# Performance work log

Hardware: AMD Instinct MI355X
Metric: run time of the kernel (lower is better)

The kernel has to match this reference:

```python
import jax, jax.numpy as jnp
import numpy as np

E, T, A, H = 64, 128, 32, 4
S, O, QH1, QD, C1 = 256, 128, 128, 64, 128  # state, obs, query hidden, query/key dim, c hidden


def setup_inputs() -> dict:
    key = jax.random.key(0)
    ks = jax.random.split(key, 10)
    w = 0.02
    return {
        "q_values": jax.random.normal(ks[0], (E, T, A), jnp.float32),
        "states": jax.random.normal(ks[1], (E, T, S), jnp.float32),
        "individual_fs": jax.random.normal(ks[2], (E, T, A, O), jnp.float32),
        "Wq1": jax.random.normal(ks[3], (S, QH1), jnp.float32) * w,
        "bq1": jnp.zeros((QH1,), jnp.float32),
        "Wq2": jax.random.normal(ks[4], (QH1, QD), jnp.float32) * w,
        "bq2": jnp.zeros((QD,), jnp.float32),
        "Wk": jax.random.normal(ks[5], (H, O, QD), jnp.float32) * w,
        "bk": jnp.zeros((H, QD), jnp.float32),
        "Wc1": jax.random.normal(ks[6], (S, C1), jnp.float32) * w,
        "bc1": jnp.zeros((C1,), jnp.float32),
        "Wc2": jax.random.normal(ks[7], (C1, 1), jnp.float32) * w,
        "bc2": jnp.zeros((1,), jnp.float32),
    }


def reference(q_values, states, individual_fs, Wq1, bq1, Wq2, bq2, Wk, bk, Wc1, bc1, Wc2, bc2):
    e, t, a = q_values.shape
    s = states.reshape(-1, states.shape[-1])              # (B, S), B = E*T
    f = individual_fs.reshape(e * t, a, -1)               # (B, A, O)
    # query embedding of state: 2-layer MLP with ReLU
    emb_s = jnp.maximum(s @ Wq1 + bq1, 0.0) @ Wq2 + bq2   # (B, QD)
    # all-agents, all-heads key extraction in one batched einsum
    emb_u = jnp.einsum('bao,hok->bahk', f, Wk) + bk       # (B, A, H, QD)
    # query-key dot products per agent/head, then sum over heads
    Lambda_i = jnp.einsum('bk,bahk->bah', emb_s, emb_u).sum(axis=-1)  # (B, A)
    # state-dependent scalar bias
    c_value = jnp.maximum(s @ Wc1 + bc1, 0.0) @ Wc2 + bc2  # (B, 1)
    Q_tot = jnp.sum(Lambda_i * q_values.reshape(-1, a), axis=-1, keepdims=True) + c_value
    return Q_tot.reshape(e, t, 1)
```

## Files before the change

### kernel.cpp

```cpp
#include <hip/hip_runtime.h>


static constexpr int Sd  = 256;
static constexpr int Ad  = 32;
static constexpr int Od  = 128;
static constexpr int QDd = 64;
static constexpr int NB  = 8;
static constexpr int NBLK = 1024;

__global__ void qatten_prep(const float* __restrict__ Wk, const float* __restrict__ bk,
                            float* __restrict__ WkT, float* __restrict__ bkSum)
{
    int idx = blockIdx.x * 256 + threadIdx.x;
    int k = idx >> 7;
    int o = idx & 127;
    float s = 0.f;
#pragma unroll
    for (int h = 0; h < 4; ++h) s += Wk[h * (Od * QDd) + o * QDd + k];
    WkT[k * Od + o] = s;
    if (idx < QDd) {
        float t = 0.f;
#pragma unroll
        for (int h = 0; h < 4; ++h) t += bk[h * QDd + idx];
        bkSum[idx] = t;
    }
}

union SEmb {
    float s[NB][Sd];
    float emb[NB][68];
};

__global__ __launch_bounds__(256, 5) void qatten_fused(
    const float* __restrict__ qv, const float* __restrict__ st, const float* __restrict__ fs,
    const float* __restrict__ Wq1, const float* __restrict__ bq1,
    const float* __restrict__ Wq2, const float* __restrict__ bq2,
    const float* __restrict__ Wc1, const float* __restrict__ bc1,
    const float* __restrict__ Wc2, const float* __restrict__ bc2,
    const float* __restrict__ WkT, const float* __restrict__ bkSum,
    float* __restrict__ out)
{
    __shared__ SEmb u;
    __shared__ float h_lds[NB][260];
    __shared__ float g_lds[NB][128];

    const int tid = threadIdx.x;
    const int b0 = blockIdx.x * NB;

    {
        const int w = tid >> 6;
        const int l = tid & 63;
        const int r0 = b0 + 2 * w;
        const float4* __restrict__ f0 = (const float4*)fs + (size_t)r0 * (Ad * Od / 4);
        const float4* __restrict__ f1 = f0 + (Ad * Od / 4);
        const float q0 = qv[(size_t)r0 * Ad + (l & 31)];
        const float q1 = qv[(size_t)(r0 + 1) * Ad + (l & 31)];
        float4 a0 = {0.f, 0.f, 0.f, 0.f}, a1 = {0.f, 0.f, 0.f, 0.f};
#pragma unroll
        for (int batch = 0; batch < 2; ++batch) {
            float4 x0[8], x1[8];
#pragma unroll
            for (int i = 0; i < 8; ++i) {
                x0[i] = f0[(batch * 8 + i) * 64 + l];
                x1[i] = f1[(batch * 8 + i) * 64 + l];
            }
#pragma unroll
            for (int i = 0; i < 8; ++i) {
                const int ii = batch * 8 + i;
                const float qa0 = __shfl(q0, 2 * ii + (l >> 5), 64);
                const float qa1 = __shfl(q1, 2 * ii + (l >> 5), 64);
                a0.x = fmaf(qa0, x0[i].x, a0.x);
                a0.y = fmaf(qa0, x0[i].y, a0.y);
                a0.z = fmaf(qa0, x0[i].z, a0.z);
                a0.w = fmaf(qa0, x0[i].w, a0.w);
                a1.x = fmaf(qa1, x1[i].x, a1.x);
                a1.y = fmaf(qa1, x1[i].y, a1.y);
                a1.z = fmaf(qa1, x1[i].z, a1.z);
                a1.w = fmaf(qa1, x1[i].w, a1.w);
            }
        }
        a0.x += __shfl_xor(a0.x, 32, 64);
        a0.y += __shfl_xor(a0.y, 32, 64);
        a0.z += __shfl_xor(a0.z, 32, 64);
        a0.w += __shfl_xor(a0.w, 32, 64);
        a1.x += __shfl_xor(a1.x, 32, 64);
        a1.y += __shfl_xor(a1.y, 32, 64);
        a1.z += __shfl_xor(a1.z, 32, 64);
        a1.w += __shfl_xor(a1.w, 32, 64);
        if (l < 32) {
            *(float4*)&g_lds[2 * w][l * 4]     = a0;
            *(float4*)&g_lds[2 * w + 1][l * 4] = a1;
        }
    }

    {
        const float4* sp = (const float4*)(st + (size_t)b0 * Sd);
        float4* sl = (float4*)&u.s[0][0];
        sl[tid]       = sp[tid];
        sl[tid + 256] = sp[tid + 256];
    }
    __syncthreads();

    {
        const int wg = tid & 63;
        const int rg = (tid >> 6) << 1;
        const float* __restrict__ Wb = (wg < 32) ? (Wq1 + 4 * wg)
                                                 : (Wc1 + 4 * (wg - 32));
        const float4 bb4 = (wg < 32) ? *(const float4*)&bq1[4 * wg]
                                     : *(const float4*)&bc1[4 * (wg - 32)];
        float acc[2][4];
#pragma unroll
        for (int r = 0; r < 2; ++r)
#pragma unroll
            for (int c = 0; c < 4; ++c) acc[r][c] = 0.f;

        for (int k = 0; k < Sd; k += 4) {
            float w[4][4];
#pragma unroll
            for (int kk = 0; kk < 4; ++kk) {
                const float4 t = *(const float4*)&Wb[(size_t)(k + kk) * 128];
                w[kk][0] = t.x; w[kk][1] = t.y; w[kk][2] = t.z; w[kk][3] = t.w;
            }
#pragma unroll
            for (int r = 0; r < 2; ++r) {
                const float4 s4 = *(const float4*)&u.s[rg + r][k];
                float a0 = acc[r][0], a1 = acc[r][1], a2 = acc[r][2], a3 = acc[r][3];
                a0 = fmaf(s4.x, w[0][0], a0); a1 = fmaf(s4.x, w[0][1], a1);
                a2 = fmaf(s4.x, w[0][2], a2); a3 = fmaf(s4.x, w[0][3], a3);
                a0 = fmaf(s4.y, w[1][0], a0); a1 = fmaf(s4.y, w[1][1], a1);
                a2 = fmaf(s4.y, w[1][2], a2); a3 = fmaf(s4.y, w[1][3], a3);
                a0 = fmaf(s4.z, w[2][0], a0); a1 = fmaf(s4.z, w[2][1], a1);
                a2 = fmaf(s4.z, w[2][2], a2); a3 = fmaf(s4.z, w[2][3], a3);
                a0 = fmaf(s4.w, w[3][0], a0); a1 = fmaf(s4.w, w[3][1], a1);
                a2 = fmaf(s4.w, w[3][2], a2); a3 = fmaf(s4.w, w[3][3], a3);
                acc[r][0] = a0; acc[r][1] = a1; acc[r][2] = a2; acc[r][3] = a3;
            }
        }
#pragma unroll
        for (int r = 0; r < 2; ++r) {
            float4 o;
            o.x = fmaxf(acc[r][0] + bb4.x, 0.f);
            o.y = fmaxf(acc[r][1] + bb4.y, 0.f);
            o.z = fmaxf(acc[r][2] + bb4.z, 0.f);
            o.w = fmaxf(acc[r][3] + bb4.w, 0.f);
            *(float4*)&h_lds[rg + r][4 * wg] = o;
        }
    }
    __syncthreads();

    {
        const int c2  = tid & 31;
        const int row = tid >> 5;
        float a0 = 0.f, a1 = 0.f;
        for (int k = 0; k < 128; k += 4) {
            float2 w[4];
#pragma unroll
            for (int kk = 0; kk < 4; ++kk)
                w[kk] = *(const float2*)&Wq2[(size_t)(k + kk) * 64 + 2 * c2];
            const float4 h4 = *(const float4*)&h_lds[row][k];
            a0 = fmaf(h4.x, w[0].x, a0);  a1 = fmaf(h4.x, w[0].y, a1);
            a0 = fmaf(h4.y, w[1].x, a0);  a1 = fmaf(h4.y, w[1].y, a1);
            a0 = fmaf(h4.z, w[2].x, a0);  a1 = fmaf(h4.z, w[2].y, a1);
            a0 = fmaf(h4.w, w[3].x, a0);  a1 = fmaf(h4.w, w[3].y, a1);
        }
        const float2 b2 = *(const float2*)&bq2[2 * c2];
        float2 o; o.x = a0 + b2.x; o.y = a1 + b2.y;
        *(float2*)&u.emb[row][2 * c2] = o;
    }
    __syncthreads();

    {
        const int cg  = tid & 31;
        const int row = tid >> 5;
        const int b   = b0 + row;

        float acc[4] = {0.f, 0.f, 0.f, 0.f};
        for (int k = 0; k < QDd; k += 4) {
            float w[4][4];
#pragma unroll
            for (int kk = 0; kk < 4; ++kk) {
                const float4 t = *(const float4*)&WkT[(size_t)(k + kk) * 128 + 4 * cg];
                w[kk][0] = t.x; w[kk][1] = t.y; w[kk][2] = t.z; w[kk][3] = t.w;
            }
            const float4 e4 = *(const float4*)&u.emb[row][k];
#pragma unroll
            for (int c = 0; c < 4; ++c) {
                float a = acc[c];
                a = fmaf(e4.x, w[0][c], a);
                a = fmaf(e4.y, w[1][c], a);
                a = fmaf(e4.z, w[2][c], a);
                a = fmaf(e4.w, w[3][c], a);
                acc[c] = a;
            }
        }
        const float4 g4 = *(const float4*)&g_lds[row][4 * cg];
        float d = acc[0] * g4.x;
        d = fmaf(acc[1], g4.y, d);
        d = fmaf(acc[2], g4.z, d);
        d = fmaf(acc[3], g4.w, d);
        float pb = fmaf(u.emb[row][cg],      bkSum[cg],      0.f);
        pb       = fmaf(u.emb[row][cg + 32], bkSum[cg + 32], pb);
        float pc = 0.f;
#pragma unroll
        for (int j = 0; j < 4; ++j)
            pc = fmaf(h_lds[row][128 + cg + 32 * j], Wc2[cg + 32 * j], pc);
        float pq = qv[(size_t)b * Ad + cg];
#pragma unroll
        for (int dd = 16; dd >= 1; dd >>= 1) {
            d  += __shfl_down(d,  dd, 32);
            pb += __shfl_down(pb, dd, 32);
            pc += __shfl_down(pc, dd, 32);
            pq += __shfl_down(pq, dd, 32);
        }
        if (cg == 0)
            out[b] = d + (pc + bc2[0]) + pb * pq;
    }
}

extern "C" void kernel_launch(void* const* d_in, const int* in_sizes, int n_in,
                              void* d_out, int out_size, void* d_ws, size_t ws_size,
                              hipStream_t stream) {
    const float* qv  = (const float*)d_in[0];
    const float* st  = (const float*)d_in[1];
    const float* fs  = (const float*)d_in[2];
    const float* Wq1 = (const float*)d_in[3];
    const float* bq1 = (const float*)d_in[4];
    const float* Wq2 = (const float*)d_in[5];
    const float* bq2 = (const float*)d_in[6];
    const float* Wk  = (const float*)d_in[7];
    const float* bk  = (const float*)d_in[8];
    const float* Wc1 = (const float*)d_in[9];
    const float* bc1 = (const float*)d_in[10];
    const float* Wc2 = (const float*)d_in[11];
    const float* bc2 = (const float*)d_in[12];
    float* out = (float*)d_out;

    float* WkT   = (float*)d_ws;
    float* bkSum = WkT + QDd * Od;

    qatten_prep<<<32, 256, 0, stream>>>(Wk, bk, WkT, bkSum);
    qatten_fused<<<NBLK, 256, 0, stream>>>(qv, st, fs, Wq1, bq1, Wq2, bq2,
                                           Wc1, bc1, Wc2, bc2, WkT, bkSum, out);
}
```

Baseline: 269.9 us.

## Warp-specialize fused kernel: producer waves stream fs while compute waves run MLP

```diff
diff --git a/kernel.cpp b/kernel.cpp
--- a/kernel.cpp
+++ b/kernel.cpp
@@ -5,8 +5,8 @@
 static constexpr int Ad  = 32;
 static constexpr int Od  = 128;
 static constexpr int QDd = 64;
-static constexpr int NB  = 8;
-static constexpr int NBLK = 1024;
+static constexpr int NB  = 16;
+static constexpr int NBLK = 512;
 
 __global__ void qatten_prep(const float* __restrict__ Wk, const float* __restrict__ bk,
                             float* __restrict__ WkT, float* __restrict__ bkSum)
@@ -26,12 +26,7 @@
     }
 }
 
-union SEmb {
-    float s[NB][Sd];
-    float emb[NB][68];
-};
-
-__global__ __launch_bounds__(256, 5) void qatten_fused(
+__global__ __launch_bounds__(512) void qatten_fused(
     const float* __restrict__ qv, const float* __restrict__ st, const float* __restrict__ fs,
     const float* __restrict__ Wq1, const float* __restrict__ bq1,
     const float* __restrict__ Wq2, const float* __restrict__ bq2,
@@ -40,180 +35,190 @@
     const float* __restrict__ WkT, const float* __restrict__ bkSum,
     float* __restrict__ out)
 {
-    __shared__ SEmb u;
+    __shared__ float s_lds[NB][Sd];
     __shared__ float h_lds[NB][260];
+    __shared__ float emb_lds[NB][68];
     __shared__ float g_lds[NB][128];
 
-    const int tid = threadIdx.x;
-    const int b0 = blockIdx.x * NB;
-
-    {
-        const int w = tid >> 6;
-        const int l = tid & 63;
-        const int r0 = b0 + 2 * w;
-        const float4* __restrict__ f0 = (const float4*)fs + (size_t)r0 * (Ad * Od / 4);
-        const float4* __restrict__ f1 = f0 + (Ad * Od / 4);
-        const float q0 = qv[(size_t)r0 * Ad + (l & 31)];
-        const float q1 = qv[(size_t)(r0 + 1) * Ad + (l & 31)];
-        float4 a0 = {0.f, 0.f, 0.f, 0.f}, a1 = {0.f, 0.f, 0.f, 0.f};
-#pragma unroll
-        for (int batch = 0; batch < 2; ++batch) {
-            float4 x0[8], x1[8];
-#pragma unroll
-            for (int i = 0; i < 8; ++i) {
-                x0[i] = f0[(batch * 8 + i) * 64 + l];
-                x1[i] = f1[(batch * 8 + i) * 64 + l];
-            }
-#pragma unroll
-            for (int i = 0; i < 8; ++i) {
-                const int ii = batch * 8 + i;
-                const float qa0 = __shfl(q0, 2 * ii + (l >> 5), 64);
-                const float qa1 = __shfl(q1, 2 * ii + (l >> 5), 64);
-                a0.x = fmaf(qa0, x0[i].x, a0.x);
-                a0.y = fmaf(qa0, x0[i].y, a0.y);
-                a0.z = fmaf(qa0, x0[i].z, a0.z);
-                a0.w = fmaf(qa0, x0[i].w, a0.w);
-                a1.x = fmaf(qa1, x1[i].x, a1.x);
-                a1.y = fmaf(qa1, x1[i].y, a1.y);
-                a1.z = fmaf(qa1, x1[i].z, a1.z);
-                a1.w = fmaf(qa1, x1[i].w, a1.w);
-            }
-        }
-        a0.x += __shfl_xor(a0.x, 32, 64);
-        a0.y += __shfl_xor(a0.y, 32, 64);
-        a0.z += __shfl_xor(a0.z, 32, 64);
-        a0.w += __shfl_xor(a0.w, 32, 64);
-        a1.x += __shfl_xor(a1.x, 32, 64);
-        a1.y += __shfl_xor(a1.y, 32, 64);
-        a1.z += __shfl_xor(a1.z, 32, 64);
-        a1.w += __shfl_xor(a1.w, 32, 64);
-        if (l < 32) {
-            *(float4*)&g_lds[2 * w][l * 4]     = a0;
-            *(float4*)&g_lds[2 * w + 1][l * 4] = a1;
+    const int tid  = threadIdx.x;
+    const int wave = tid >> 6;
+    const int l    = tid & 63;
+    const int b0   = blockIdx.x * NB;
+
+    float vreg[4][2];
+
+    if (wave < 4) {
+        const int r0 = b0 + 4 * wave;
+#pragma unroll
+        for (int p = 0; p < 2; ++p) {
+            const int ra = r0 + 2 * p;
+            const float4* __restrict__ f0 = (const float4*)fs + (size_t)ra * (Ad * Od / 4);
+            const float4* __restrict__ f1 = f0 + (Ad * Od / 4);
+            const float q0 = qv[(size_t)ra * Ad + (l & 31)];
+            const float q1 = qv[(size_t)(ra + 1) * Ad + (l & 31)];
+            float4 a0 = {0.f, 0.f, 0.f, 0.f}, a1 = {0.f, 0.f, 0.f, 0.f};
+#pragma unroll
+            for (int batch = 0; batch < 2; ++batch) {
+                float4 x0[8], x1[8];
+#pragma unroll
+                for (int i = 0; i < 8; ++i) {
+                    x0[i] = f0[(batch * 8 + i) * 64 + l];
+                    x1[i] = f1[(batch * 8 + i) * 64 + l];
+                }
+#pragma unroll
+                for (int i = 0; i < 8; ++i) {
+                    const int ii = batch * 8 + i;
+                    const float qa0 = __shfl(q0, 2 * ii + (l >> 5), 64);
+                    const float qa1 = __shfl(q1, 2 * ii + (l >> 5), 64);
+                    a0.x = fmaf(qa0, x0[i].x, a0.x);
+                    a0.y = fmaf(qa0, x0[i].y, a0.y);
+                    a0.z = fmaf(qa0, x0[i].z, a0.z);
+                    a0.w = fmaf(qa0, x0[i].w, a0.w);
+                    a1.x = fmaf(qa1, x1[i].x, a1.x);
+                    a1.y = fmaf(qa1, x1[i].y, a1.y);
+                    a1.z = fmaf(qa1, x1[i].z, a1.z);
+                    a1.w = fmaf(qa1, x1[i].w, a1.w);
+                }
+            }
+            a0.x += __shfl_xor(a0.x, 32, 64);
+            a0.y += __shfl_xor(a0.y, 32, 64);
+            a0.z += __shfl_xor(a0.z, 32, 64);
+            a0.w += __shfl_xor(a0.w, 32, 64);
+            a1.x += __shfl_xor(a1.x, 32, 64);
+            a1.y += __shfl_xor(a1.y, 32, 64);
+            a1.z += __shfl_xor(a1.z, 32, 64);
+            a1.w += __shfl_xor(a1.w, 32, 64);
+            if (l < 32) {
+                *(float4*)&g_lds[4 * wave + 2 * p][l * 4]     = a0;
+                *(float4*)&g_lds[4 * wave + 2 * p + 1][l * 4] = a1;
+            }
+        }
+    } else {
+        const int m  = wave - 4;
+        const int lr = 4 * m;
+
+        {
+            const float4* sp = (const float4*)(st + (size_t)(b0 + lr) * Sd);
+            float4* sl = (float4*)&s_lds[lr][0];
+#pragma unroll
+            for (int i = 0; i < 4; ++i) sl[l + 64 * i] = sp[l + 64 * i];
+        }
+
+        {
+            const float* __restrict__ Wb = (l < 32) ? (Wq1 + 4 * l)
+                                                    : (Wc1 + 4 * (l - 32));
+            const float4 bb4 = (l < 32) ? *(const float4*)&bq1[4 * l]
+                                        : *(const float4*)&bc1[4 * (l - 32)];
+            float acc[4][4];
+#pragma unroll
+            for (int r = 0; r < 4; ++r)
+#pragma unroll
+                for (int c = 0; c < 4; ++c) acc[r][c] = 0.f;
+
+            for (int k = 0; k < Sd; k += 4) {
+                float w[4][4];
+#pragma unroll
+                for (int kk = 0; kk < 4; ++kk) {
+                    const float4 t = *(const float4*)&Wb[(size_t)(k + kk) * 128];
+                    w[kk][0] = t.x; w[kk][1] = t.y; w[kk][2] = t.z; w[kk][3] = t.w;
+                }
+#pragma unroll
+                for (int r = 0; r < 4; ++r) {
+                    const float4 s4 = *(const float4*)&s_lds[lr + r][k];
+                    float a0 = acc[r][0], a1 = acc[r][1], a2 = acc[r][2], a3 = acc[r][3];
+                    a0 = fmaf(s4.x, w[0][0], a0); a1 = fmaf(s4.x, w[0][1], a1);
+                    a2 = fmaf(s4.x, w[0][2], a2); a3 = fmaf(s4.x, w[0][3], a3);
+                    a0 = fmaf(s4.y, w[1][0], a0); a1 = fmaf(s4.y, w[1][1], a1);
+                    a2 = fmaf(s4.y, w[1][2], a2); a3 = fmaf(s4.y, w[1][3], a3);
+                    a0 = fmaf(s4.z, w[2][0], a0); a1 = fmaf(s4.z, w[2][1], a1);
+                    a2 = fmaf(s4.z, w[2][2], a2); a3 = fmaf(s4.z, w[2][3], a3);
+                    a0 = fmaf(s4.w, w[3][0], a0); a1 = fmaf(s4.w, w[3][1], a1);
+                    a2 = fmaf(s4.w, w[3][2], a2); a3 = fmaf(s4.w, w[3][3], a3);
+                    acc[r][0] = a0; acc[r][1] = a1; acc[r][2] = a2; acc[r][3] = a3;
+                }
+            }
+#pragma unroll
+            for (int r = 0; r < 4; ++r) {
+                float4 o;
+                o.x = fmaxf(acc[r][0] + bb4.x, 0.f);
+                o.y = fmaxf(acc[r][1] + bb4.y, 0.f);
+                o.z = fmaxf(acc[r][2] + bb4.z, 0.f);
+                o.w = fmaxf(acc[r][3] + bb4.w, 0.f);
+                *(float4*)&h_lds[lr + r][4 * l] = o;
+            }
+        }
+
+        {
+            float e[4] = {0.f, 0.f, 0.f, 0.f};
+            for (int k = 0; k < 128; k += 4) {
+                const float w0 = Wq2[(size_t)(k + 0) * 64 + l];
+                const float w1 = Wq2[(size_t)(k + 1) * 64 + l];
+                const float w2 = Wq2[(size_t)(k + 2) * 64 + l];
+                const float w3 = Wq2[(size_t)(k + 3) * 64 + l];
+#pragma unroll
+                for (int r = 0; r < 4; ++r) {
+                    const float4 h4 = *(const float4*)&h_lds[lr + r][k];
+                    float a = e[r];
+                    a = fmaf(h4.x, w0, a);
+                    a = fmaf(h4.y, w1, a);
+                    a = fmaf(h4.z, w2, a);
+                    a = fmaf(h4.w, w3, a);
+                    e[r] = a;
+                }
+            }
+            const float bq = bq2[l];
+#pragma unroll
+            for (int r = 0; r < 4; ++r) emb_lds[lr + r][l] = e[r] + bq;
+        }
+
+        {
+#pragma unroll
+            for (int r = 0; r < 4; ++r) { vreg[r][0] = 0.f; vreg[r][1] = 0.f; }
+            for (int k = 0; k < QDd; k += 4) {
+                float wA[4], wB[4];
+#pragma unroll
+                for (int kk = 0; kk < 4; ++kk) {
+                    wA[kk] = WkT[(size_t)(k + kk) * 128 + l];
+                    wB[kk] = WkT[(size_t)(k + kk) * 128 + 64 + l];
+                }
+#pragma unroll
+                for (int r = 0; r < 4; ++r) {
+                    const float4 e4 = *(const float4*)&emb_lds[lr + r][k];
+                    float a = vreg[r][0], b = vreg[r][1];
+                    a = fmaf(e4.x, wA[0], a);  b = fmaf(e4.x, wB[0], b);
+                    a = fmaf(e4.y, wA[1], a);  b = fmaf(e4.y, wB[1], b);
+                    a = fmaf(e4.z, wA[2], a);  b = fmaf(e4.z, wB[2], b);
+                    a = fmaf(e4.w, wA[3], a);  b = fmaf(e4.w, wB[3], b);
+                    vreg[r][0] = a; vreg[r][1] = b;
+                }
+            }
         }
     }
 
-    {
-        const float4* sp = (const float4*)(st + (size_t)b0 * Sd);
-        float4* sl = (float4*)&u.s[0][0];
-        sl[tid]       = sp[tid];
-        sl[tid + 256] = sp[tid + 256];
-    }
     __syncthreads();
 
-    {
-        const int wg = tid & 63;
-        const int rg = (tid >> 6) << 1;
-        const float* __restrict__ Wb = (wg < 32) ? (Wq1 + 4 * wg)
-                                                 : (Wc1 + 4 * (wg - 32));
-        const float4 bb4 = (wg < 32) ? *(const float4*)&bq1[4 * wg]
-                                     : *(const float4*)&bc1[4 * (wg - 32)];
-        float acc[2][4];
-#pragma unroll
-        for (int r = 0; r < 2; ++r)
-#pragma unroll
-            for (int c = 0; c < 4; ++c) acc[r][c] = 0.f;
-
-        for (int k = 0; k < Sd; k += 4) {
-            float w[4][4];
-#pragma unroll
-            for (int kk = 0; kk < 4; ++kk) {
-                const float4 t = *(const float4*)&Wb[(size_t)(k + kk) * 128];
-                w[kk][0] = t.x; w[kk][1] = t.y; w[kk][2] = t.z; w[kk][3] = t.w;
-            }
-#pragma unroll
-            for (int r = 0; r < 2; ++r) {
-                const float4 s4 = *(const float4*)&u.s[rg + r][k];
-                float a0 = acc[r][0], a1 = acc[r][1], a2 = acc[r][2], a3 = acc[r][3];
-                a0 = fmaf(s4.x, w[0][0], a0); a1 = fmaf(s4.x, w[0][1], a1);
-                a2 = fmaf(s4.x, w[0][2], a2); a3 = fmaf(s4.x, w[0][3], a3);
-                a0 = fmaf(s4.y, w[1][0], a0); a1 = fmaf(s4.y, w[1][1], a1);
-                a2 = fmaf(s4.y, w[1][2], a2); a3 = fmaf(s4.y, w[1][3], a3);
-                a0 = fmaf(s4.z, w[2][0], a0); a1 = fmaf(s4.z, w[2][1], a1);
-                a2 = fmaf(s4.z, w[2][2], a2); a3 = fmaf(s4.z, w[2][3], a3);
-                a0 = fmaf(s4.w, w[3][0], a0); a1 = fmaf(s4.w, w[3][1], a1);
-                a2 = fmaf(s4.w, w[3][2], a2); a3 = fmaf(s4.w, w[3][3], a3);
-                acc[r][0] = a0; acc[r][1] = a1; acc[r][2] = a2; acc[r][3] = a3;
-            }
-        }
-#pragma unroll
-        for (int r = 0; r < 2; ++r) {
-            float4 o;
-            o.x = fmaxf(acc[r][0] + bb4.x, 0.f);
-            o.y = fmaxf(acc[r][1] + bb4.y, 0.f);
-            o.z = fmaxf(acc[r][2] + bb4.z, 0.f);
-            o.w = fmaxf(acc[r][3] + bb4.w, 0.f);
-            *(float4*)&h_lds[rg + r][4 * wg] = o;
-        }
-    }
-    __syncthreads();
-
-    {
-        const int c2  = tid & 31;
-        const int row = tid >> 5;
-        float a0 = 0.f, a1 = 0.f;
-        for (int k = 0; k < 128; k += 4) {
-            float2 w[4];
-#pragma unroll
-            for (int kk = 0; kk < 4; ++kk)
-                w[kk] = *(const float2*)&Wq2[(size_t)(k + kk) * 64 + 2 * c2];
-            const float4 h4 = *(const float4*)&h_lds[row][k];
-            a0 = fmaf(h4.x, w[0].x, a0);  a1 = fmaf(h4.x, w[0].y, a1);
-            a0 = fmaf(h4.y, w[1].x, a0);  a1 = fmaf(h4.y, w[1].y, a1);
-            a0 = fmaf(h4.z, w[2].x, a0);  a1 = fmaf(h4.z, w[2].y, a1);
-            a0 = fmaf(h4.w, w[3].x, a0);  a1 = fmaf(h4.w, w[3].y, a1);
-        }
-        const float2 b2 = *(const float2*)&bq2[2 * c2];
-        float2 o; o.x = a0 + b2.x; o.y = a1 + b2.y;
-        *(float2*)&u.emb[row][2 * c2] = o;
-    }
-    __syncthreads();
-
-    {
-        const int cg  = tid & 31;
-        const int row = tid >> 5;
-        const int b   = b0 + row;
-
-        float acc[4] = {0.f, 0.f, 0.f, 0.f};
-        for (int k = 0; k < QDd; k += 4) {
-            float w[4][4];
-#pragma unroll
-            for (int kk = 0; kk < 4; ++kk) {
-                const float4 t = *(const float4*)&WkT[(size_t)(k + kk) * 128 + 4 * cg];
-                w[kk][0] = t.x; w[kk][1] = t.y; w[kk][2] = t.z; w[kk][3] = t.w;
-            }
-            const float4 e4 = *(const float4*)&u.emb[row][k];
-#pragma unroll
-            for (int c = 0; c < 4; ++c) {
-                float a = acc[c];
-                a = fmaf(e4.x, w[0][c], a);
-                a = fmaf(e4.y, w[1][c], a);
-                a = fmaf(e4.z, w[2][c], a);
-                a = fmaf(e4.w, w[3][c], a);
-                acc[c] = a;
-            }
-        }
-        const float4 g4 = *(const float4*)&g_lds[row][4 * cg];
-        float d = acc[0] * g4.x;
-        d = fmaf(acc[1], g4.y, d);
-        d = fmaf(acc[2], g4.z, d);
-        d = fmaf(acc[3], g4.w, d);
-        float pb = fmaf(u.emb[row][cg],      bkSum[cg],      0.f);
-        pb       = fmaf(u.emb[row][cg + 32], bkSum[cg + 32], pb);
-        float pc = 0.f;
-#pragma unroll
-        for (int j = 0; j < 4; ++j)
-            pc = fmaf(h_lds[row][128 + cg + 32 * j], Wc2[cg + 32 * j], pc);
-        float pq = qv[(size_t)b * Ad + cg];
-#pragma unroll
-        for (int dd = 16; dd >= 1; dd >>= 1) {
-            d  += __shfl_down(d,  dd, 32);
-            pb += __shfl_down(pb, dd, 32);
-            pc += __shfl_down(pc, dd, 32);
-            pq += __shfl_down(pq, dd, 32);
-        }
-        if (cg == 0)
-            out[b] = d + (pc + bc2[0]) + pb * pq;
+    if (wave >= 4) {
+        const int lr = 4 * (wave - 4);
+        const float wc2a = Wc2[l], wc2b = Wc2[l + 64];
+        const float bks  = bkSum[l];
+#pragma unroll
+        for (int r = 0; r < 4; ++r) {
+            const int row = lr + r;
+            const int b   = b0 + row;
+            float e = vreg[r][0] * g_lds[row][l];
+            e = fmaf(vreg[r][1], g_lds[row][l + 64], e);
+            e = fmaf(h_lds[row][128 + l], wc2a, e);
+            e = fmaf(h_lds[row][192 + l], wc2b, e);
+            float pb = emb_lds[row][l] * bks;
+            float pq = (l < 32) ? qv[(size_t)b * Ad + l] : 0.f;
+#pragma unroll
+            for (int d = 32; d >= 1; d >>= 1) {
+                e  += __shfl_xor(e,  d, 64);
+                pb += __shfl_xor(pb, d, 64);
+                pq += __shfl_xor(pq, d, 64);
+            }
+            if (l == 0) out[b] = e + bc2[0] + pb * pq;
+        }
     }
 }
 
@@ -239,6 +244,6 @@
     float* bkSum = WkT + QDd * Od;
 
     qatten_prep<<<32, 256, 0, stream>>>(Wk, bk, WkT, bkSum);
-    qatten_fused<<<NBLK, 256, 0, stream>>>(qv, st, fs, Wq1, bq1, Wq2, bq2,
+    qatten_fused<<<NBLK, 512, 0, stream>>>(qv, st, fs, Wq1, bq1, Wq2, bq2,
                                            Wc1, bc1, Wc2, bc2, WkT, bkSum, out);
 }
```

Measured after the change: 243.2 us. -9.9%, faster.
